# Optimization experiments

Hardware: AMD Instinct MI355X
Metric: run time of the kernel (lower is better)

Reference implementation:

```python
import jax, jax.numpy as jnp
import numpy as np

L = 16
IN0 = 7  # 3 + 3 + 1 per the torch module
CH = [16, 32, 16]
N = 500000
NEG_SLOPE = 0.2


def setup_inputs() -> dict:
    key = jax.random.key(0)
    ks = jax.random.split(key, 5)
    x = jax.random.normal(ks[0], (N, IN0), dtype=jnp.float32)
    idx = jax.random.randint(ks[1], (N,), 0, L, dtype=jnp.int32)
    # kaiming-uniform-like init scale per layer fan-in
    def init_w(k, shape):
        fan_in = shape[1]
        bound = float(np.sqrt(6.0 / fan_in))
        return jax.random.uniform(k, shape, dtype=jnp.float32, minval=-bound, maxval=bound)
    W0 = init_w(ks[2], (L, IN0, CH[0]))
    W1 = init_w(ks[3], (L, CH[0], CH[1]))
    W2 = init_w(ks[4], (L, CH[1], CH[2]))
    b0 = jnp.zeros((L, CH[0]), dtype=jnp.float32)
    b1 = jnp.zeros((L, CH[1]), dtype=jnp.float32)
    b2 = jnp.zeros((L, CH[2]), dtype=jnp.float32)
    return {"x": x, "idx": idx, "W0": W0, "b0": b0, "W1": W1, "b1": b1, "W2": W2, "b2": b2}


def reference(x, idx, W0, b0, W1, b1, W2, b2):
    # Per-point expert-indexed MLP: h <- LeakyReLU(h @ W[idx] + b[idx]) per layer.
    h = x
    for W, b in ((W0, b0), (W1, b1), (W2, b2)):
        # gather per-point weight [N, in, out] and bias [N, out], vec-mat per point
        h = jax.nn.leaky_relu(
            jnp.einsum("nc,nco->no", h, W[idx]) + b[idx],
            negative_slope=NEG_SLOPE,
        )
    return h
```

## Files before the change

kernel.cpp:

```cpp
#include <hip/hip_runtime.h>
#include <hip/hip_fp16.h>


#define L_EXP 16
#define IN0   7
#define C0    16
#define C1    32
#define C2    16
#define NEG   0.2f
#define BLK   256
#define MPT   4
#define SEGPAD (BLK * MPT)
#define CHUNK  1024
#define NBM    512

#define NW0T 2048
#define NW1T 8192
#define NW2T 8192
#define NWT_TOT (NW0T + NW1T + NW2T)
#define PREPBLK (NWT_TOT / BLK)

#define WS_PART  64
#define WB_W0T   33792
#define WB_W1T   37888
#define WB_W2T   54272
#define WS_PERM  18432

typedef _Float16 h2 __attribute__((ext_vector_type(2)));
union F4H { float4 f4; h2 h[4]; };

__device__ __forceinline__ h2 pk(float a, float b) {
    return __builtin_bit_cast(h2, __builtin_amdgcn_cvt_pkrtz(a, b));
}

__global__ void k_hist(const int* __restrict__ idx, int n, int nblk,
                       int* __restrict__ ws,
                       const float* __restrict__ W0,
                       const float* __restrict__ W1,
                       const float* __restrict__ W2) {
    int t = threadIdx.x;
    if (blockIdx.x >= nblk) {
        int k = (blockIdx.x - nblk) * BLK + t;
        __half* hW0 = (__half*)((char*)ws + WB_W0T);
        __half* hW1 = (__half*)((char*)ws + WB_W1T);
        __half* hW2 = (__half*)((char*)ws + WB_W2T);
        if (k < NW0T) {
            int e = k >> 7, r = k & 127, o = r >> 3, c = r & 7;
            float v = (c < IN0) ? W0[e * (IN0 * C0) + c * C0 + o] : 0.0f;
            hW0[k] = __float2half(v);
        } else if (k < NW0T + NW1T) {
            int k2 = k - NW0T;
            int e = k2 >> 9, r = k2 & 511, o = r >> 4, c = r & 15;
            hW1[k2] = __float2half(W1[e * (C0 * C1) + c * C1 + o]);
        } else {
            int k2 = k - NW0T - NW1T;
            int e = k2 >> 9, r = k2 & 511, o = r >> 5, c = r & 31;
            hW2[k2] = __float2half(W2[e * (C1 * C2) + c * C2 + o]);
        }
        return;
    }
    __shared__ int bins[L_EXP];
    if (t < L_EXP) bins[t] = 0;
    __syncthreads();
    int i4 = blockIdx.x * CHUNK + t * 4;
    if (i4 + 3 < n) {
        int4 v = *reinterpret_cast<const int4*>(idx + i4);
        atomicAdd(&bins[v.x & 15], 1);
        atomicAdd(&bins[v.y & 15], 1);
        atomicAdd(&bins[v.z & 15], 1);
        atomicAdd(&bins[v.w & 15], 1);
    } else {
#pragma unroll
        for (int q = 0; q < 4; ++q)
            if (i4 + q < n) atomicAdd(&bins[idx[i4 + q] & 15], 1);
    }
    __syncthreads();
    if (t < L_EXP) ws[WS_PART + t * NBM + blockIdx.x] = bins[t];
}

__global__ void k_scan(int* __restrict__ ws, int nblk) {
    int t = threadIdx.x;
    int e = t >> 6, l = t & 63;
    int running = 0;
    for (int c = 0; c < nblk; c += 64) {
        int b = c + l;
        int v = (b < nblk) ? ws[WS_PART + e * NBM + b] : 0;
        int s = v;
#pragma unroll
        for (int d = 1; d < 64; d <<= 1) {
            int u = __shfl_up(s, d, 64);
            if (l >= d) s += u;
        }
        if (b < nblk) ws[WS_PART + e * NBM + b] = running + (s - v);
        running += __shfl(s, 63, 64);
    }
    if (l == 0) ws[e] = running;
    __syncthreads();
    if (t == 0) {
        int run = 0;
        for (int q = 0; q < L_EXP; ++q) {
            ws[16 + q] = run;
            run += ((ws[q] + SEGPAD - 1) / SEGPAD) * SEGPAD;
        }
        ws[32] = run;
    }
}

__global__ void k_scatter(const int* __restrict__ idx, int n,
                          int* __restrict__ ws) {
    __shared__ int soff[L_EXP];
    __shared__ int lcount[L_EXP];
    int t = threadIdx.x;
    if (t < L_EXP) {
        soff[t] = ws[16 + t] + ws[WS_PART + t * NBM + blockIdx.x];
        lcount[t] = 0;
    }
    __syncthreads();
    int i4 = blockIdx.x * CHUNK + t * 4;
#pragma unroll
    for (int q = 0; q < 4; ++q) {
        int i = i4 + q;
        if (i < n) {
            int e = idx[i] & 15;
            int r = atomicAdd(&lcount[e], 1);
            ws[WS_PERM + soff[e] + r] = i;
        }
    }
}

__device__ __forceinline__ float leaky(float a) { return fmaxf(a, NEG * a); }

__device__ __forceinline__ float fdot2(h2 a, h2 b, float c) {
    return __builtin_amdgcn_fdot2(a, b, c, false);
}

__global__ void __launch_bounds__(BLK, 2) k_mlp(
    const int* __restrict__ meta, const float* __restrict__ x,
    const float* __restrict__ b0, const float* __restrict__ b1,
    const float* __restrict__ b2, float* __restrict__ out) {
    __shared__ __align__(16) __half sW0t[C0 * 8];
    __shared__ __align__(16) __half sW1t[C1 * C0];
    __shared__ __align__(16) __half sW2t[C2 * C1];
    __shared__ __align__(16) float sB0[C0];
    __shared__ __align__(16) float sB1[C1];
    __shared__ __align__(16) float sB2[C2];

    int start = blockIdx.x * SEGPAD;
    if (start >= meta[32]) return;

    int e = 0;
    while (start >= meta[16 + e + 1]) ++e;
    e = __builtin_amdgcn_readfirstlane(e);

    int t = threadIdx.x;
    {
        const int* w0i = (const int*)((const char*)meta + WB_W0T) + e * 64;
        const int* w1i = (const int*)((const char*)meta + WB_W1T) + e * 256;
        const int* w2i = (const int*)((const char*)meta + WB_W2T) + e * 256;
        if (t < 64) reinterpret_cast<int*>(sW0t)[t] = w0i[t];
        reinterpret_cast<int*>(sW1t)[t] = w1i[t];
        reinterpret_cast<int*>(sW2t)[t] = w2i[t];
        if (t >= 128 && t < 128 + C0) sB0[t - 128] = b0[e * C0 + (t - 128)];
        if (t >= 160 && t < 160 + C1) sB1[t - 160] = b1[e * C1 + (t - 160)];
        if (t >= 192 && t < 192 + C2) sB2[t - 192] = b2[e * C2 + (t - 192)];
    }
    __syncthreads();

    int seg = meta[16 + e];
    int cnt = meta[e];
    int j0 = start - seg + t;

    h2  xh[MPT][4];
    int pid[MPT];
    bool act[MPT];
#pragma unroll
    for (int m = 0; m < MPT; ++m) {
        int j = j0 + m * BLK;
        act[m] = (j < cnt);
        int p = meta[WS_PERM + seg + j];
        pid[m] = act[m] ? p : 0;
        const float* xp = x + (size_t)pid[m] * IN0;
        float4 a = *reinterpret_cast<const float4*>(xp);
        float4 b = *reinterpret_cast<const float4*>(xp + 3);
        xh[m][0] = pk(a.x, a.y);
        xh[m][1] = pk(a.z, a.w);
        xh[m][2] = pk(b.y, b.z);
        xh[m][3] = pk(b.w, 0.0f);
    }
    __builtin_amdgcn_sched_barrier(0);

    float h0f[MPT][C0];
#pragma unroll
    for (int o = 0; o < C0; ++o) {
        F4H u;
        u.f4 = *reinterpret_cast<const float4*>(&sW0t[o * 8]);
#pragma unroll
        for (int m = 0; m < MPT; ++m) {
            float a = sB0[o];
            a = fdot2(xh[m][0], u.h[0], a);
            a = fdot2(xh[m][1], u.h[1], a);
            a = fdot2(xh[m][2], u.h[2], a);
            a = fdot2(xh[m][3], u.h[3], a);
            h0f[m][o] = leaky(a);
        }
        if (o == 7) __builtin_amdgcn_sched_barrier(0);
    }
    h2 h0h[MPT][8];
#pragma unroll
    for (int m = 0; m < MPT; ++m)
#pragma unroll
        for (int p = 0; p < 8; ++p)
            h0h[m][p] = pk(h0f[m][2 * p], h0f[m][2 * p + 1]);
    __builtin_amdgcn_sched_barrier(0);

    float h2a[MPT][C2];
#pragma unroll
    for (int m = 0; m < MPT; ++m)
#pragma unroll
        for (int o = 0; o < C2; ++o) h2a[m][o] = sB2[o];
#pragma unroll 1
    for (int ch = 0; ch < C1 / 8; ++ch) {
        float tvf[MPT][8];
#pragma unroll
        for (int o8 = 0; o8 < 8; ++o8) {
            int o = ch * 8 + o8;
            F4H ua, ub;
            ua.f4 = reinterpret_cast<const float4*>(&sW1t[o * C0])[0];
            ub.f4 = reinterpret_cast<const float4*>(&sW1t[o * C0])[1];
#pragma unroll
            for (int m = 0; m < MPT; ++m) {
                float a = sB1[o];
                a = fdot2(h0h[m][0], ua.h[0], a);
                a = fdot2(h0h[m][1], ua.h[1], a);
                a = fdot2(h0h[m][2], ua.h[2], a);
                a = fdot2(h0h[m][3], ua.h[3], a);
                a = fdot2(h0h[m][4], ub.h[0], a);
                a = fdot2(h0h[m][5], ub.h[1], a);
                a = fdot2(h0h[m][6], ub.h[2], a);
                a = fdot2(h0h[m][7], ub.h[3], a);
                tvf[m][o8] = leaky(a);
            }
        }
        __builtin_amdgcn_sched_barrier(0);
        h2 tvh[MPT][4];
#pragma unroll
        for (int m = 0; m < MPT; ++m)
#pragma unroll
            for (int p = 0; p < 4; ++p)
                tvh[m][p] = pk(tvf[m][2 * p], tvf[m][2 * p + 1]);
#pragma unroll
        for (int o = 0; o < C2; ++o) {
            F4H u;
            u.f4 = *reinterpret_cast<const float4*>(&sW2t[o * C1 + ch * 8]);
#pragma unroll
            for (int m = 0; m < MPT; ++m) {
                float a = h2a[m][o];
                a = fdot2(tvh[m][0], u.h[0], a);
                a = fdot2(tvh[m][1], u.h[1], a);
                a = fdot2(tvh[m][2], u.h[2], a);
                a = fdot2(tvh[m][3], u.h[3], a);
                h2a[m][o] = a;
            }
        }
        __builtin_amdgcn_sched_barrier(0);
    }

#pragma unroll
    for (int m = 0; m < MPT; ++m) {
        if (act[m]) {
            float4* outp = reinterpret_cast<float4*>(out + (size_t)pid[m] * C2);
#pragma unroll
            for (int og = 0; og < C2 / 4; ++og) {
                float4 o;
                o.x = leaky(h2a[m][og * 4 + 0]);
                o.y = leaky(h2a[m][og * 4 + 1]);
                o.z = leaky(h2a[m][og * 4 + 2]);
                o.w = leaky(h2a[m][og * 4 + 3]);
                outp[og] = o;
            }
        }
    }
}

extern "C" void kernel_launch(void* const* d_in, const int* in_sizes, int n_in,
                              void* d_out, int out_size, void* d_ws, size_t ws_size,
                              hipStream_t stream) {
    const float* x  = (const float*)d_in[0];
    const int*  idx = (const int*)d_in[1];
    const float* W0 = (const float*)d_in[2];
    const float* b0 = (const float*)d_in[3];
    const float* W1 = (const float*)d_in[4];
    const float* b1 = (const float*)d_in[5];
    const float* W2 = (const float*)d_in[6];
    const float* b2 = (const float*)d_in[7];
    float* out = (float*)d_out;

    int n = in_sizes[1];
    int* ws = (int*)d_ws;

    int nblk = (n + CHUNK - 1) / CHUNK;
    k_hist<<<nblk + PREPBLK, BLK, 0, stream>>>(idx, n, nblk, ws, W0, W1, W2);
    k_scan<<<1, 1024, 0, stream>>>(ws, nblk);
    k_scatter<<<nblk, BLK, 0, stream>>>(idx, n, ws);

    int mblk = (n + L_EXP * (SEGPAD - 1) + SEGPAD - 1) / SEGPAD;
    k_mlp<<<mblk, BLK, 0, stream>>>(ws, x, b0, b1, b2, out);
}
```

Measured before the change: 116.2 us.

## Fuse histogram, scan and scatter into one cooperative kernel with grid syncs

Measured after the change: 358.5 us. +208.4%, slower.

```diff
diff --git a/kernel.cpp b/kernel.cpp
--- a/kernel.cpp
+++ b/kernel.cpp
@@ -1,5 +1,8 @@
 #include <hip/hip_runtime.h>
 #include <hip/hip_fp16.h>
+#include <hip/hip_cooperative_groups.h>
+
+namespace cg = cooperative_groups;
 
 
 #define L_EXP 16
@@ -33,97 +36,127 @@
     return __builtin_bit_cast(h2, __builtin_amdgcn_cvt_pkrtz(a, b));
 }
 
-__global__ void k_hist(const int* __restrict__ idx, int n, int nblk,
-                       int* __restrict__ ws,
-                       const float* __restrict__ W0,
-                       const float* __restrict__ W1,
-                       const float* __restrict__ W2) {
+__global__ void k_pre(const int* __restrict__ idx, int n, int nblk,
+                      int* __restrict__ ws,
+                      const float* __restrict__ W0,
+                      const float* __restrict__ W1,
+                      const float* __restrict__ W2) {
+    cg::grid_group grid = cg::this_grid();
     int t = threadIdx.x;
-    if (blockIdx.x >= nblk) {
-        int k = (blockIdx.x - nblk) * BLK + t;
-        __half* hW0 = (__half*)((char*)ws + WB_W0T);
-        __half* hW1 = (__half*)((char*)ws + WB_W1T);
-        __half* hW2 = (__half*)((char*)ws + WB_W2T);
-        if (k < NW0T) {
-            int e = k >> 7, r = k & 127, o = r >> 3, c = r & 7;
-            float v = (c < IN0) ? W0[e * (IN0 * C0) + c * C0 + o] : 0.0f;
-            hW0[k] = __float2half(v);
-        } else if (k < NW0T + NW1T) {
-            int k2 = k - NW0T;
-            int e = k2 >> 9, r = k2 & 511, o = r >> 4, c = r & 15;
-            hW1[k2] = __float2half(W1[e * (C0 * C1) + c * C1 + o]);
-        } else {
-            int k2 = k - NW0T - NW1T;
-            int e = k2 >> 9, r = k2 & 511, o = r >> 5, c = r & 31;
-            hW2[k2] = __float2half(W2[e * (C1 * C2) + c * C2 + o]);
-        }
-        return;
-    }
+    int b = blockIdx.x;
+
     __shared__ int bins[L_EXP];
+    __shared__ int wsum[4];
+    __shared__ int soff[L_EXP];
+    __shared__ int lcount[L_EXP];
+
     if (t < L_EXP) bins[t] = 0;
     __syncthreads();
-    int i4 = blockIdx.x * CHUNK + t * 4;
+
+    int i4 = b * CHUNK + t * 4;
+    int4 v = make_int4(-1, -1, -1, -1);
     if (i4 + 3 < n) {
-        int4 v = *reinterpret_cast<const int4*>(idx + i4);
+        v = *reinterpret_cast<const int4*>(idx + i4);
         atomicAdd(&bins[v.x & 15], 1);
         atomicAdd(&bins[v.y & 15], 1);
         atomicAdd(&bins[v.z & 15], 1);
         atomicAdd(&bins[v.w & 15], 1);
     } else {
-#pragma unroll
-        for (int q = 0; q < 4; ++q)
-            if (i4 + q < n) atomicAdd(&bins[idx[i4 + q] & 15], 1);
+        int q0 = (i4 + 0 < n) ? idx[i4 + 0] : -1;
+        int q1 = (i4 + 1 < n) ? idx[i4 + 1] : -1;
+        int q2 = (i4 + 2 < n) ? idx[i4 + 2] : -1;
+        int q3 = (i4 + 3 < n) ? idx[i4 + 3] : -1;
+        v = make_int4(q0, q1, q2, q3);
+        if (q0 >= 0) atomicAdd(&bins[q0 & 15], 1);
+        if (q1 >= 0) atomicAdd(&bins[q1 & 15], 1);
+        if (q2 >= 0) atomicAdd(&bins[q2 & 15], 1);
+        if (q3 >= 0) atomicAdd(&bins[q3 & 15], 1);
     }
     __syncthreads();
-    if (t < L_EXP) ws[WS_PART + t * NBM + blockIdx.x] = bins[t];
-}
-
-__global__ void k_scan(int* __restrict__ ws, int nblk) {
-    int t = threadIdx.x;
-    int e = t >> 6, l = t & 63;
-    int running = 0;
-    for (int c = 0; c < nblk; c += 64) {
-        int b = c + l;
-        int v = (b < nblk) ? ws[WS_PART + e * NBM + b] : 0;
-        int s = v;
-#pragma unroll
-        for (int d = 1; d < 64; d <<= 1) {
+    if (t < L_EXP) ws[WS_PART + t * NBM + b] = bins[t];
+
+    {
+        __half* hW0 = (__half*)((char*)ws + WB_W0T);
+        __half* hW1 = (__half*)((char*)ws + WB_W1T);
+        __half* hW2 = (__half*)((char*)ws + WB_W2T);
+        for (int kb = b; kb < PREPBLK; kb += nblk) {
+            int k = kb * BLK + t;
+            if (k < NW0T) {
+                int e = k >> 7, r = k & 127, o = r >> 3, c = r & 7;
+                float w = (c < IN0) ? W0[e * (IN0 * C0) + c * C0 + o] : 0.0f;
+                hW0[k] = __float2half(w);
+            } else if (k < NW0T + NW1T) {
+                int k2 = k - NW0T;
+                int e = k2 >> 9, r = k2 & 511, o = r >> 4, c = r & 15;
+                hW1[k2] = __float2half(W1[e * (C0 * C1) + c * C1 + o]);
+            } else {
+                int k2 = k - NW0T - NW1T;
+                int e = k2 >> 9, r = k2 & 511, o = r >> 5, c = r & 31;
+                hW2[k2] = __float2half(W2[e * (C1 * C2) + c * C2 + o]);
+            }
+        }
+    }
+    __threadfence();
+    grid.sync();
+
+    if (b < L_EXP) {
+        int e = b;
+        int wid = t >> 6, lane = t & 63;
+        int running = 0;
+        for (int c = 0; c < nblk; c += BLK) {
+            int bb = c + t;
+            int pv = (bb < nblk) ? ws[WS_PART + e * NBM + bb] : 0;
+            int s = pv;
+#pragma unroll
+            for (int d = 1; d < 64; d <<= 1) {
+                int u = __shfl_up(s, d, 64);
+                if (lane >= d) s += u;
+            }
+            if (lane == 63) wsum[wid] = s;
+            __syncthreads();
+            int off = 0;
+#pragma unroll
+            for (int w = 0; w < 4; ++w)
+                if (w < wid) off += wsum[w];
+            if (bb < nblk) ws[WS_PART + e * NBM + bb] = running + off + (s - pv);
+            int tot = wsum[0] + wsum[1] + wsum[2] + wsum[3];
+            __syncthreads();
+            running += tot;
+        }
+        if (t == 0) ws[e] = running;
+    }
+    __threadfence();
+    grid.sync();
+
+    if (b == 0 && t < L_EXP) {
+        int cnt = ws[t];
+        int pad = ((cnt + SEGPAD - 1) / SEGPAD) * SEGPAD;
+        int s = pad;
+#pragma unroll
+        for (int d = 1; d < L_EXP; d <<= 1) {
             int u = __shfl_up(s, d, 64);
-            if (l >= d) s += u;
-        }
-        if (b < nblk) ws[WS_PART + e * NBM + b] = running + (s - v);
-        running += __shfl(s, 63, 64);
-    }
-    if (l == 0) ws[e] = running;
+            if (t >= d) s += u;
+        }
+        ws[16 + t] = s - pad;
+        if (t == L_EXP - 1) ws[32] = s;
+    }
+    __threadfence();
+    grid.sync();
+
+    if (t < L_EXP) {
+        soff[t] = ws[16 + t] + ws[WS_PART + t * NBM + b];
+        lcount[t] = 0;
+    }
     __syncthreads();
-    if (t == 0) {
-        int run = 0;
-        for (int q = 0; q < L_EXP; ++q) {
-            ws[16 + q] = run;
-            run += ((ws[q] + SEGPAD - 1) / SEGPAD) * SEGPAD;
-        }
-        ws[32] = run;
-    }
-}
-
-__global__ void k_scatter(const int* __restrict__ idx, int n,
-                          int* __restrict__ ws) {
-    __shared__ int soff[L_EXP];
-    __shared__ int lcount[L_EXP];
-    int t = threadIdx.x;
-    if (t < L_EXP) {
-        soff[t] = ws[16 + t] + ws[WS_PART + t * NBM + blockIdx.x];
-        lcount[t] = 0;
-    }
-    __syncthreads();
-    int i4 = blockIdx.x * CHUNK + t * 4;
-#pragma unroll
-    for (int q = 0; q < 4; ++q) {
-        int i = i4 + q;
-        if (i < n) {
-            int e = idx[i] & 15;
-            int r = atomicAdd(&lcount[e], 1);
-            ws[WS_PERM + soff[e] + r] = i;
+    {
+        int q[4] = {v.x, v.y, v.z, v.w};
+#pragma unroll
+        for (int m = 0; m < 4; ++m) {
+            if (q[m] >= 0) {
+                int e = q[m] & 15;
+                int r = atomicAdd(&lcount[e], 1);
+                ws[WS_PERM + soff[e] + r] = i4 + m;
+            }
         }
     }
 }
@@ -299,9 +332,11 @@
     int* ws = (int*)d_ws;
 
     int nblk = (n + CHUNK - 1) / CHUNK;
-    k_hist<<<nblk + PREPBLK, BLK, 0, stream>>>(idx, n, nblk, ws, W0, W1, W2);
-    k_scan<<<1, 1024, 0, stream>>>(ws, nblk);
-    k_scatter<<<nblk, BLK, 0, stream>>>(idx, n, ws);
+
+    void* args[] = {(void*)&idx, (void*)&n, (void*)&nblk, (void*)&ws,
+                    (void*)&W0, (void*)&W1, (void*)&W2};
+    hipLaunchCooperativeKernel((const void*)k_pre, dim3(nblk), dim3(BLK),
+                               args, 0, stream);
 
     int mblk = (n + L_EXP * (SEGPAD - 1) + SEGPAD - 1) / SEGPAD;
     k_mlp<<<mblk, BLK, 0, stream>>>(ws, x, b0, b1, b2, out);
```

## Fold the single-block scan kernel into the scatter kernel

Applied to the files above, without the earlier changes.

After: 117.8 us. About the same (+1.3%).

```diff
diff --git a/kernel.cpp b/kernel.cpp
--- a/kernel.cpp
+++ b/kernel.cpp
@@ -78,45 +78,49 @@
     if (t < L_EXP) ws[WS_PART + t * NBM + blockIdx.x] = bins[t];
 }
 
-__global__ void k_scan(int* __restrict__ ws, int nblk) {
-    int t = threadIdx.x;
-    int e = t >> 6, l = t & 63;
-    int running = 0;
-    for (int c = 0; c < nblk; c += 64) {
-        int b = c + l;
-        int v = (b < nblk) ? ws[WS_PART + e * NBM + b] : 0;
-        int s = v;
-#pragma unroll
-        for (int d = 1; d < 64; d <<= 1) {
-            int u = __shfl_up(s, d, 64);
-            if (l >= d) s += u;
-        }
-        if (b < nblk) ws[WS_PART + e * NBM + b] = running + (s - v);
-        running += __shfl(s, 63, 64);
-    }
-    if (l == 0) ws[e] = running;
-    __syncthreads();
-    if (t == 0) {
-        int run = 0;
-        for (int q = 0; q < L_EXP; ++q) {
-            ws[16 + q] = run;
-            run += ((ws[q] + SEGPAD - 1) / SEGPAD) * SEGPAD;
-        }
-        ws[32] = run;
-    }
-}
-
-__global__ void k_scatter(const int* __restrict__ idx, int n,
+__global__ void k_scatter(const int* __restrict__ idx, int n, int nblk,
                           int* __restrict__ ws) {
+    __shared__ int pre_s[L_EXP][17];
+    __shared__ int tot_s[L_EXP][17];
     __shared__ int soff[L_EXP];
     __shared__ int lcount[L_EXP];
     int t = threadIdx.x;
+    int b = blockIdx.x;
+
+    {
+        int e = t & 15, j = t >> 4;
+        int pre = 0, tot = 0;
+        for (int bb = j; bb < nblk; bb += 16) {
+            int v = ws[WS_PART + e * NBM + bb];
+            tot += v;
+            if (bb < b) pre += v;
+        }
+        pre_s[e][j] = pre;
+        tot_s[e][j] = tot;
+    }
+    __syncthreads();
     if (t < L_EXP) {
-        soff[t] = ws[16 + t] + ws[WS_PART + t * NBM + blockIdx.x];
+        int pre = 0, tot = 0;
+#pragma unroll
+        for (int q = 0; q < 16; ++q) { pre += pre_s[t][q]; tot += tot_s[t][q]; }
+        int pad = ((tot + SEGPAD - 1) / SEGPAD) * SEGPAD;
+        int s = pad;
+#pragma unroll
+        for (int d = 1; d < L_EXP; d <<= 1) {
+            int u = __shfl_up(s, d, 64);
+            if (t >= d) s += u;
+        }
+        int segoff = s - pad;
+        soff[t] = segoff + pre;
         lcount[t] = 0;
-    }
-    __syncthreads();
-    int i4 = blockIdx.x * CHUNK + t * 4;
+        if (b == 0) {
+            ws[t] = tot;
+            ws[16 + t] = segoff;
+            if (t == L_EXP - 1) ws[32] = s;
+        }
+    }
+    __syncthreads();
+    int i4 = b * CHUNK + t * 4;
 #pragma unroll
     for (int q = 0; q < 4; ++q) {
         int i = i4 + q;
@@ -300,8 +304,7 @@
 
     int nblk = (n + CHUNK - 1) / CHUNK;
     k_hist<<<nblk + PREPBLK, BLK, 0, stream>>>(idx, n, nblk, ws, W0, W1, W2);
-    k_scan<<<1, 1024, 0, stream>>>(ws, nblk);
-    k_scatter<<<nblk, BLK, 0, stream>>>(idx, n, ws);
+    k_scatter<<<nblk, BLK, 0, stream>>>(idx, n, nblk, ws);
 
     int mblk = (n + L_EXP * (SEGPAD - 1) + SEGPAD - 1) / SEGPAD;
     k_mlp<<<mblk, BLK, 0, stream>>>(ws, x, b0, b1, b2, out);
```
